# Kernel tuning notes

Hardware: AMD Instinct MI355X
Metric: run time of the kernel (lower is better)

Reference implementation:

```python
import jax, jax.numpy as jnp
import numpy as np

N_EMBD = 2560
N_HEAD = 32
HEAD_DIM = N_EMBD // N_HEAD  # 80
ROTARY_DIM = 32
SEQ = 2048
BSZ = 1


def _rope_tables(seq_len, rotary_dim, base=10000.0):
    inv_freq = 1.0 / (base ** (np.arange(0, rotary_dim, 2, dtype=np.float32) / rotary_dim))
    t = np.arange(seq_len, dtype=np.float32)
    freqs = np.outer(t, inv_freq)                      # [S, rd/2]
    emb = np.concatenate([freqs, freqs], axis=-1)      # [S, rd]
    return jnp.asarray(np.cos(emb)), jnp.asarray(np.sin(emb))


def setup_inputs() -> dict:
    key = jax.random.key(0)
    k1, k2, k3, k4, k5 = jax.random.split(key, 5)
    op_size = HEAD_DIM * (N_HEAD + 2 * N_HEAD)  # fused q,k,v => 3*n_embd
    hidden_states = jax.random.normal(k1, (BSZ, SEQ, N_EMBD), dtype=jnp.float32)
    Wqkv_w = jax.random.normal(k2, (op_size, N_EMBD), dtype=jnp.float32) * 0.02
    Wqkv_b = jax.random.normal(k3, (op_size,), dtype=jnp.float32) * 0.02
    out_w = jax.random.normal(k4, (N_EMBD, N_EMBD), dtype=jnp.float32) * 0.02
    out_b = jax.random.normal(k5, (N_EMBD,), dtype=jnp.float32) * 0.02
    cos, sin = _rope_tables(SEQ, ROTARY_DIM)
    return {"hidden_states": hidden_states, "Wqkv_w": Wqkv_w, "Wqkv_b": Wqkv_b,
            "out_w": out_w, "out_b": out_b, "cos": cos, "sin": sin}


def apply_partial_rotary(x, cos, sin):
    # x: [S, B, H, D]; cos/sin: [S, rd]
    rd = cos.shape[-1]
    c = cos[:, None, None, :]
    s = sin[:, None, None, :]
    x_rot = x[..., :rd]
    # NOTE: faithful to source -- rotated half is concatenated WITHOUT negation
    tmp = jnp.concatenate([x[..., rd // 2:rd], x[..., :rd // 2]], axis=-1)
    rotten = x_rot * c + tmp * s
    return jnp.concatenate([rotten, x[..., rd:]], axis=-1)


def reference(hidden_states, Wqkv_w, Wqkv_b, out_w, out_b, cos, sin):
    bsz, q_len, _ = hidden_states.shape
    qkv = hidden_states @ Wqkv_w.T + Wqkv_b            # [B, S, 3*E]
    q, k, v = jnp.split(qkv, 3, axis=-1)
    # [B, S, H, D] -> [S, B, H, D] for rotary
    q = q.reshape(bsz, q_len, N_HEAD, HEAD_DIM).transpose(1, 0, 2, 3)
    k = k.reshape(bsz, q_len, N_HEAD, HEAD_DIM).transpose(1, 0, 2, 3)
    v = v.reshape(bsz, q_len, N_HEAD, HEAD_DIM).transpose(0, 2, 1, 3)  # [B, H, S, D]
    cos_t, sin_t = cos[:q_len], sin[:q_len]
    q = apply_partial_rotary(q, cos_t, sin_t).transpose(1, 2, 0, 3)    # [B, H, S, D]
    k = apply_partial_rotary(k, cos_t, sin_t).transpose(1, 2, 0, 3)    # [B, H, S, D]
    scale = 1.0 / jnp.sqrt(jnp.asarray(HEAD_DIM, dtype=q.dtype))
    scores = jnp.einsum('bhqd,bhkd->bhqk', q, k) * scale
    causal = jnp.tril(jnp.ones((q_len, q_len), dtype=bool))
    scores = jnp.where(causal, scores, jnp.asarray(-1e30, dtype=scores.dtype))
    probs = jax.nn.softmax(scores, axis=-1)
    out = jnp.einsum('bhqk,bhkd->bhqd', probs, v)       # [B, H, S, D]
    out = out.transpose(0, 2, 1, 3).reshape(bsz, q_len, N_EMBD)
    return out @ out_w.T + out_b
```

## Files before the change

kernel.cpp:

```cpp
#include <hip/hip_runtime.h>
#include <cstdint>
#include <cstddef>

typedef unsigned short bf16_t;
typedef __attribute__((ext_vector_type(8))) short bf16x8;
typedef __attribute__((ext_vector_type(4))) float f32x4;

__device__ __forceinline__ float bf2f(bf16_t b) {
  unsigned int u = ((unsigned int)b) << 16;
  return __builtin_bit_cast(float, u);
}
__device__ __forceinline__ bf16_t f2bf(float f) {
  unsigned int u = __builtin_bit_cast(unsigned int, f);
  u += 0x7fffu + ((u >> 16) & 1u);
  return (bf16_t)(u >> 16);
}
__device__ __forceinline__ float exp2_hw(float x) {
  return __builtin_amdgcn_exp2f(x);
}

constexpr int SEQ = 2048, NE = 2560, NH = 32, HD = 80, OP = 7680;

__global__ void cvt3(const float* __restrict__ s0, const float* __restrict__ s1,
                     const float* __restrict__ s2, bf16_t* __restrict__ d0,
                     bf16_t* __restrict__ d1, bf16_t* __restrict__ d2)
{
  constexpr int N0 = SEQ * NE / 4, N1 = OP * NE / 4;
  int t = blockIdx.x * 256 + threadIdx.x;
  const float* s; bf16_t* d;
  if (t < N0)            { s = s0; d = d0; }
  else if (t < N0 + N1)  { s = s1; d = d1; t -= N0; }
  else                   { s = s2; d = d2; t -= N0 + N1; }
  float4 v = ((const float4*)s)[t];
  ushort4 o;
  o.x = f2bf(v.x); o.y = f2bf(v.y); o.z = f2bf(v.z); o.w = f2bf(v.w);
  ((ushort4*)d)[t] = o;
}

__device__ __forceinline__ void store_out(bf16_t* p, float v) { *p = f2bf(v); }
__device__ __forceinline__ void store_out(float* p, float v)  { *p = v; }

__global__ __launch_bounds__(512, 2) void gemm256_bt_bias(
    const bf16_t* __restrict__ A,
    const bf16_t* __restrict__ B,
    const float*  __restrict__ bias,
    bf16_t* __restrict__ C,
    int M, int N, int K)
{
  __shared__ bf16_t As[2][256 * 64];
  __shared__ bf16_t Bs[2][256 * 64];

  const int tid  = threadIdx.x;
  const int lane = tid & 63;
  const int wave = tid >> 6;
  const int wm   = wave >> 2;
  const int wn   = wave & 3;
  const int lm   = lane & 15;
  const int quad = lane >> 4;
  const int m0 = blockIdx.y * 256;
  const int n0 = blockIdx.x * 256;
  const int NT = K / 64;

  const int srow = lane >> 3;
  const int scol = ((lane & 7) ^ srow) * 8;

  auto stage = [&](const bf16_t* __restrict__ P, int R0, int K0, int H, bf16_t* DST) {
#pragma unroll
    for (int cc = 0; cc < 2; ++cc) {
      const int seg = wave * 2 + cc;
      const bf16_t* src = P + (size_t)(R0 + H * 128 + seg * 8 + srow) * K + K0 + scol;
      __builtin_amdgcn_global_load_lds(
          (const __attribute__((address_space(1))) unsigned int*)src,
          (__attribute__((address_space(3))) unsigned int*)(DST + H * 8192 + seg * 512),
          16, 0, 0);
    }
  };

  const int xk0 = ((0 + quad) ^ (lm & 7)) * 8;
  const int xk1 = ((4 + quad) ^ (lm & 7)) * 8;

  f32x4 acc[8][4];
#pragma unroll
  for (int i = 0; i < 8; ++i)
#pragma unroll
    for (int j = 0; j < 4; ++j)
      acc[i][j] = (f32x4){0.f, 0.f, 0.f, 0.f};

  stage(A, m0, 0, 0, As[0]);  stage(A, m0, 0, 1, As[0]);
  stage(B, n0, 0, 0, Bs[0]);  stage(B, n0, 0, 1, Bs[0]);
  stage(B, n0, 64, 0, Bs[1]); stage(B, n0, 64, 1, Bs[1]);
  stage(A, m0, 64, 0, As[1]); stage(A, m0, 64, 1, As[1]);

  for (int t = 0; t < NT; ++t) {
    const int c = t & 1;
    const bf16_t* Ab = &As[c][(wm * 128 + lm) * 64];
    const bf16_t* Bb = &Bs[c][(wn * 64 + lm) * 64];

    if (t == NT - 1) asm volatile("s_waitcnt vmcnt(0)" ::: "memory");
    else             asm volatile("s_waitcnt vmcnt(8)" ::: "memory");
    __builtin_amdgcn_s_barrier();

    bf16x8 a[4][2], b01[2][2], b23[2][2];

#pragma unroll
    for (int i = 0; i < 4; ++i) {
      a[i][0] = *(const bf16x8*)(Ab + i * 1024 + xk0);
      a[i][1] = *(const bf16x8*)(Ab + i * 1024 + xk1);
    }
#pragma unroll
    for (int j = 0; j < 2; ++j) {
      b01[j][0] = *(const bf16x8*)(Bb + j * 1024 + xk0);
      b01[j][1] = *(const bf16x8*)(Bb + j * 1024 + xk1);
    }
    __builtin_amdgcn_s_barrier();
    asm volatile("s_waitcnt lgkmcnt(0)" ::: "memory");
    __builtin_amdgcn_sched_barrier(0);
    __builtin_amdgcn_s_setprio(1);
#pragma unroll
    for (int kk = 0; kk < 2; ++kk)
#pragma unroll
      for (int i = 0; i < 4; ++i)
#pragma unroll
        for (int j = 0; j < 2; ++j)
          acc[i][j] = __builtin_amdgcn_mfma_f32_16x16x32_bf16(a[i][kk], b01[j][kk], acc[i][j], 0, 0, 0);
    __builtin_amdgcn_s_setprio(0);
    __builtin_amdgcn_s_barrier();

#pragma unroll
    for (int j = 0; j < 2; ++j) {
      b23[j][0] = *(const bf16x8*)(Bb + (2 + j) * 1024 + xk0);
      b23[j][1] = *(const bf16x8*)(Bb + (2 + j) * 1024 + xk1);
    }
    __builtin_amdgcn_s_barrier();
    asm volatile("s_waitcnt lgkmcnt(0)" ::: "memory");
    __builtin_amdgcn_sched_barrier(0);
    __builtin_amdgcn_s_setprio(1);
#pragma unroll
    for (int kk = 0; kk < 2; ++kk)
#pragma unroll
      for (int i = 0; i < 4; ++i)
#pragma unroll
        for (int j = 0; j < 2; ++j)
          acc[i][2 + j] = __builtin_amdgcn_mfma_f32_16x16x32_bf16(a[i][kk], b23[j][kk], acc[i][2 + j], 0, 0, 0);
    __builtin_amdgcn_s_setprio(0);
    __builtin_amdgcn_s_barrier();

#pragma unroll
    for (int i = 0; i < 4; ++i) {
      a[i][0] = *(const bf16x8*)(Ab + (4 + i) * 1024 + xk0);
      a[i][1] = *(const bf16x8*)(Ab + (4 + i) * 1024 + xk1);
    }
    if (t + 2 < NT) {
      stage(B, n0, (t + 2) * 64, 0, (bf16_t*)Bs[c]);
      stage(B, n0, (t + 2) * 64, 1, (bf16_t*)Bs[c]);
    }
    __builtin_amdgcn_s_barrier();
    asm volatile("s_waitcnt lgkmcnt(0)" ::: "memory");
    __builtin_amdgcn_sched_barrier(0);
    __builtin_amdgcn_s_setprio(1);
#pragma unroll
    for (int kk = 0; kk < 2; ++kk)
#pragma unroll
      for (int i = 0; i < 4; ++i)
#pragma unroll
        for (int j = 0; j < 2; ++j)
          acc[4 + i][j] = __builtin_amdgcn_mfma_f32_16x16x32_bf16(a[i][kk], b01[j][kk], acc[4 + i][j], 0, 0, 0);
    __builtin_amdgcn_s_setprio(0);
    __builtin_amdgcn_s_barrier();

    if (t + 2 < NT) {
      stage(A, m0, (t + 2) * 64, 0, (bf16_t*)As[c]);
      stage(A, m0, (t + 2) * 64, 1, (bf16_t*)As[c]);
    }
    __builtin_amdgcn_s_barrier();
    __builtin_amdgcn_s_setprio(1);
#pragma unroll
    for (int kk = 0; kk < 2; ++kk)
#pragma unroll
      for (int i = 0; i < 4; ++i)
#pragma unroll
        for (int j = 0; j < 2; ++j)
          acc[4 + i][2 + j] = __builtin_amdgcn_mfma_f32_16x16x32_bf16(a[i][kk], b23[j][kk], acc[4 + i][2 + j], 0, 0, 0);
    __builtin_amdgcn_s_setprio(0);
  }

#pragma unroll
  for (int i = 0; i < 8; ++i) {
#pragma unroll
    for (int j = 0; j < 4; ++j) {
      const int n = n0 + wn * 64 + j * 16 + lm;
      const float bv = bias ? bias[n] : 0.f;
#pragma unroll
      for (int r = 0; r < 4; ++r) {
        const int m = m0 + wm * 128 + i * 16 + quad * 4 + r;
        C[(size_t)m * N + n] = f2bf(acc[i][j][r] + bv);
      }
    }
  }
}

template <typename OutT>
__global__ __launch_bounds__(256, 2) void gemm_bt_bias(
    const bf16_t* __restrict__ A,
    const bf16_t* __restrict__ B,
    const float*  __restrict__ bias,
    OutT* __restrict__ C,
    int M, int N, int K, int klen)
{
  __shared__ bf16_t As[2][128 * 32];
  __shared__ bf16_t Bs[2][128 * 32];

  const int tid  = threadIdx.x;
  const int lane = tid & 63;
  const int wave = tid >> 6;
  const int m0 = blockIdx.y * 128;
  const int n0 = blockIdx.x * 128;
  const int kbeg = blockIdx.z * klen;
  OutT* Cz = C + (size_t)blockIdx.z * M * N;
  const int mw = (wave >> 1) * 64;
  const int nw = (wave & 1) * 64;
  const int lm = lane & 15;
  const int lq = lane >> 4;

  f32x4 acc[4][4];
#pragma unroll
  for (int i = 0; i < 4; ++i)
#pragma unroll
    for (int j = 0; j < 4; ++j)
      acc[i][j] = (f32x4){0.f, 0.f, 0.f, 0.f};

  const int ldr = lane >> 2;
  const int ldc = (lane & 3) * 8;

  for (int kt = kbeg; kt < kbeg + klen; kt += 64) {
#pragma unroll
    for (int sub = 0; sub < 2; ++sub) {
#pragma unroll
      for (int r = 0; r < 2; ++r) {
        const int seg = wave * 2 + r;
        const int row = seg * 16 + ldr;
        const int col = kt + sub * 32 + ldc;
        const bf16_t* ga = A + (size_t)(m0 + row) * K + col;
        const bf16_t* gb = B + (size_t)(n0 + row) * K + col;
        __builtin_amdgcn_global_load_lds(
            (const __attribute__((address_space(1))) unsigned int*)ga,
            (__attribute__((address_space(3))) unsigned int*)&As[sub][seg * 512], 16, 0, 0);
        __builtin_amdgcn_global_load_lds(
            (const __attribute__((address_space(1))) unsigned int*)gb,
            (__attribute__((address_space(3))) unsigned int*)&Bs[sub][seg * 512], 16, 0, 0);
      }
    }
    __syncthreads();

#pragma unroll
    for (int sub = 0; sub < 2; ++sub) {
      bf16x8 af[4], bfq[4];
#pragma unroll
      for (int i = 0; i < 4; ++i)
        af[i] = *(const bf16x8*)&As[sub][(mw + i * 16 + lm) * 32 + lq * 8];
#pragma unroll
      for (int j = 0; j < 4; ++j)
        bfq[j] = *(const bf16x8*)&Bs[sub][(nw + j * 16 + lm) * 32 + lq * 8];

#pragma unroll
      for (int i = 0; i < 4; ++i)
#pragma unroll
        for (int j = 0; j < 4; ++j)
          acc[i][j] = __builtin_amdgcn_mfma_f32_16x16x32_bf16(af[i], bfq[j], acc[i][j], 0, 0, 0);
    }

    __syncthreads();
  }

#pragma unroll
  for (int i = 0; i < 4; ++i) {
#pragma unroll
    for (int j = 0; j < 4; ++j) {
      const int n = n0 + nw + j * 16 + lm;
      const float bv = bias ? bias[n] : 0.f;
#pragma unroll
      for (int r = 0; r < 4; ++r) {
        const int m = m0 + mw + i * 16 + lq * 4 + r;
        store_out(&Cz[(size_t)m * N + n], acc[i][j][r] + bv);
      }
    }
  }
}

__global__ void reduce2_bias(const float* __restrict__ p, const float* __restrict__ bias,
                             float* __restrict__ out)
{
  const int t = blockIdx.x * 256 + threadIdx.x;
  const float4 a = ((const float4*)p)[t];
  const float4 b = ((const float4*)(p + (size_t)SEQ * NE))[t];
  const float4 bv = ((const float4*)bias)[t % (NE / 4)];
  float4 r;
  r.x = a.x + b.x + bv.x; r.y = a.y + b.y + bv.y;
  r.z = a.z + b.z + bv.z; r.w = a.w + b.w + bv.w;
  ((float4*)out)[t] = r;
}

constexpr int TSTR = 82;
__global__ void rope_vtrans(bf16_t* __restrict__ qkv,
                            const float* __restrict__ cosb,
                            const float* __restrict__ sinb,
                            bf16_t* __restrict__ vtg)
{
  __shared__ bf16_t T[64 * TSTR];
  const int tid = threadIdx.x;

  if (blockIdx.x < 8192) {
    const int t = blockIdx.x * 256 + tid;
    const int i  = t & 15;
    const int qk = (t >> 4) & 1;
    const int h  = (t >> 5) & 31;
    const int s  = t >> 10;
    const size_t base = (size_t)s * OP + qk * NE + h * HD;
    const float xi = bf2f(qkv[base + i]);
    const float xj = bf2f(qkv[base + i + 16]);
    const float c1 = cosb[s * 32 + i];
    const float s1 = sinb[s * 32 + i];
    const float c2 = cosb[s * 32 + i + 16];
    const float s2 = sinb[s * 32 + i + 16];
    qkv[base + i]      = f2bf(xi * c1 + xj * s1);
    qkv[base + i + 16] = f2bf(xj * c2 + xi * s2);
    return;
  }

  const int vb = blockIdx.x - 8192;
  const int h  = vb >> 5;
  const int sb = (vb & 31) * 64;
  const int voff = 2 * NE + h * HD;

#pragma unroll
  for (int i = 0; i < 10; ++i) {
    const int u = i * 256 + tid;
    const int row = u / 40, c = u % 40;
    const unsigned int w = *(const unsigned int*)(qkv + (size_t)(sb + row) * OP + voff + 2 * c);
    *(unsigned int*)&T[row * TSTR + 2 * c] = w;
  }
  __syncthreads();

  bf16_t* vh = vtg + (size_t)h * HD * SEQ;
#pragma unroll
  for (int i = 0; i < 10; ++i) {
    const int u = i * 256 + tid;
    const int d = u >> 5, sp = u & 31;
    const unsigned int lo = T[(2 * sp) * TSTR + d];
    const unsigned int hi = T[(2 * sp + 1) * TSTR + d];
    *(unsigned int*)(vh + (size_t)d * SEQ + sb + 2 * sp) = lo | (hi << 16);
  }
}

constexpr int KSTR = 96;
constexpr int VSTR = 72;
constexpr int PSTR = 72;

__global__ __launch_bounds__(256, 4) void attn_mfma(
    const bf16_t* __restrict__ qkv, const bf16_t* __restrict__ vtg,
    bf16_t* __restrict__ aout)
{
  __shared__ bf16_t Ks[12 * 512];
  __shared__ bf16_t Vt[12 * 512];
  __shared__ bf16_t Ps[4][16 * PSTR];

  const int h    = blockIdx.y;
  const int qt   = (int)gridDim.x - 1 - blockIdx.x;
  const int q0   = qt * 64;
  const int tid  = threadIdx.x;
  const int lane = tid & 63;
  const int wave = tid >> 6;
  const int lm   = lane & 15;
  const int quad = lane >> 4;

  const int qg = q0 + 16 * wave + lm;

  const int koff = NE + h * HD;
  const bf16_t* vh = vtg + (size_t)h * HD * SEQ;
  const float EC = 0.1118033988749895f * 1.4426950408889634f;

  bf16x8 qf[3];
  {
    const bf16_t* q_r = qkv + (size_t)qg * OP + h * HD;
#pragma unroll
    for (int ks = 0; ks < 3; ++ks) {
      const int col = ks * 32 + quad * 8;
      if (col < 80) qf[ks] = *(const bf16x8*)(q_r + col);
      else          qf[ks] = (bf16x8){0,0,0,0,0,0,0,0};
    }
  }

  int kofs[3];
#pragma unroll
  for (int r = 0; r < 3; ++r) {
    const int e = (wave * 3 + r) * 512 + lane * 8;
    const int row = e / 96, c = e % 96;
    kofs[r] = row * OP + (c < 80 ? c : c - 16);
  }
  int vofs[3];
#pragma unroll
  for (int r = 0; r < 3; ++r) {
    const int e = (wave * 3 + r) * 512 + lane * 8;
    int row = e / 72;
    const int c = e % 72;
    if (row >= 80) row -= 80;
    vofs[r] = row * SEQ + (c < 64 ? c : c - 16);
  }

  f32x4 oacc[5];
#pragma unroll
  for (int mt = 0; mt < 5; ++mt) oacc[mt] = (f32x4){0.f,0.f,0.f,0.f};
  float lsum = 0.f;

  const int ntiles = qt + 1;
  for (int t = 0; t < ntiles; ++t) {
    const int kb = t * 64;

#pragma unroll
    for (int r = 0; r < 3; ++r) {
      const bf16_t* gk = qkv + (size_t)kb * OP + koff + kofs[r];
      __builtin_amdgcn_global_load_lds(
          (const __attribute__((address_space(1))) unsigned int*)gk,
          (__attribute__((address_space(3))) unsigned int*)&Ks[(wave * 3 + r) * 512],
          16, 0, 0);
      const bf16_t* gv = vh + kb + vofs[r];
      __builtin_amdgcn_global_load_lds(
          (const __attribute__((address_space(1))) unsigned int*)gv,
          (__attribute__((address_space(3))) unsigned int*)&Vt[(wave * 3 + r) * 512],
          16, 0, 0);
    }
    __syncthreads();

    f32x4 sacc[4];
#pragma unroll
    for (int mt = 0; mt < 4; ++mt) sacc[mt] = (f32x4){0.f,0.f,0.f,0.f};
#pragma unroll
    for (int ks = 0; ks < 3; ++ks) {
      bf16x8 kf[4];
#pragma unroll
      for (int mt = 0; mt < 4; ++mt)
        kf[mt] = *(const bf16x8*)&Ks[(mt * 16 + lm) * KSTR + ks * 32 + quad * 8];
#pragma unroll
      for (int mt = 0; mt < 4; ++mt)
        sacc[mt] = __builtin_amdgcn_mfma_f32_16x16x32_bf16(kf[mt], qf[ks], sacc[mt], 0, 0, 0);
    }

    if (t == ntiles - 1) {
      const int keyb = kb + quad * 4;
#pragma unroll
      for (int mt = 0; mt < 4; ++mt) {
        float ps[4];
#pragma unroll
        for (int r = 0; r < 4; ++r) {
          float p = exp2_hw(sacc[mt][r] * EC);
          p = (keyb + mt * 16 + r > qg) ? 0.f : p;
          ps[r] = p;
        }
        lsum += (ps[0] + ps[1]) + (ps[2] + ps[3]);
        ushort4 pk;
        pk.x = f2bf(ps[0]); pk.y = f2bf(ps[1]); pk.z = f2bf(ps[2]); pk.w = f2bf(ps[3]);
        *(ushort4*)&Ps[wave][lm * PSTR + mt * 16 + quad * 4] = pk;
      }
    } else {
#pragma unroll
      for (int mt = 0; mt < 4; ++mt) {
        float ps[4];
#pragma unroll
        for (int r = 0; r < 4; ++r) ps[r] = exp2_hw(sacc[mt][r] * EC);
        lsum += (ps[0] + ps[1]) + (ps[2] + ps[3]);
        ushort4 pk;
        pk.x = f2bf(ps[0]); pk.y = f2bf(ps[1]); pk.z = f2bf(ps[2]); pk.w = f2bf(ps[3]);
        *(ushort4*)&Ps[wave][lm * PSTR + mt * 16 + quad * 4] = pk;
      }
    }

#pragma unroll
    for (int ks = 0; ks < 2; ++ks) {
      bf16x8 vf[5], pf;
#pragma unroll
      for (int mt = 0; mt < 5; ++mt)
        vf[mt] = *(const bf16x8*)&Vt[(mt * 16 + lm) * VSTR + ks * 32 + quad * 8];
      pf = *(const bf16x8*)&Ps[wave][lm * PSTR + ks * 32 + quad * 8];
#pragma unroll
      for (int mt = 0; mt < 5; ++mt)
        oacc[mt] = __builtin_amdgcn_mfma_f32_16x16x32_bf16(vf[mt], pf, oacc[mt], 0, 0, 0);
    }
    __syncthreads();
  }

  lsum += __shfl_xor(lsum, 16);
  lsum += __shfl_xor(lsum, 32);
  const float inv = 1.f / lsum;
  bf16_t* base = aout + (size_t)qg * NE + h * HD + quad * 4;
#pragma unroll
  for (int mt = 0; mt < 5; ++mt) {
    ushort4 st;
    st.x = f2bf(oacc[mt][0] * inv);
    st.y = f2bf(oacc[mt][1] * inv);
    st.z = f2bf(oacc[mt][2] * inv);
    st.w = f2bf(oacc[mt][3] * inv);
    *(ushort4*)(base + mt * 16) = st;
  }
}

extern "C" void kernel_launch(void* const* d_in, const int* in_sizes, int n_in,
                              void* d_out, int out_size, void* d_ws, size_t ws_size,
                              hipStream_t stream)
{
  const float* hs   = (const float*)d_in[0];
  const float* wqkv = (const float*)d_in[1];
  const float* bqkv = (const float*)d_in[2];
  const float* wout = (const float*)d_in[3];
  const float* bout = (const float*)d_in[4];
  const float* cosb = (const float*)d_in[5];
  const float* sinb = (const float*)d_in[6];

  bf16_t* hs_bf   = (bf16_t*)d_ws;
  bf16_t* wqkv_bf = hs_bf   + (size_t)SEQ * NE;
  bf16_t* wout_bf = wqkv_bf + (size_t)OP * NE;
  bf16_t* qkv     = wout_bf + (size_t)NE * NE;
  bf16_t* aout    = qkv     + (size_t)SEQ * OP;
  float*  out     = (float*)d_out;
  bf16_t* vtg     = hs_bf;
  float*  pbuf    = (float*)d_ws;

  constexpr int CVT_T = (SEQ * NE + OP * NE + NE * NE) / 4;
  cvt3<<<CVT_T / 256, 256, 0, stream>>>(hs, wqkv, wout, hs_bf, wqkv_bf, wout_bf);

  gemm256_bt_bias<<<dim3(OP / 256, SEQ / 256), 512, 0, stream>>>(
      hs_bf, wqkv_bf, bqkv, qkv, SEQ, OP, NE);
  rope_vtrans<<<8192 + 1024, 256, 0, stream>>>(qkv, cosb, sinb, vtg);
  attn_mfma<<<dim3(SEQ / 64, NH), 256, 0, stream>>>(qkv, vtg, aout);
  gemm_bt_bias<float><<<dim3(NE / 128, SEQ / 128, 2), 256, 0, stream>>>(
      aout, wout_bf, nullptr, pbuf, SEQ, NE, NE, NE / 2);
  reduce2_bias<<<(SEQ * NE / 4) / 256, 256, 0, stream>>>(pbuf, bout, out);
}
```

Before: 390.3 us.

## Software-pipeline LDS fragment loads in GEMM main loop and cut barriers

```diff
diff --git a/kernel.cpp b/kernel.cpp
--- a/kernel.cpp
+++ b/kernel.cpp
@@ -79,6 +79,9 @@
   const int xk0 = ((0 + quad) ^ (lm & 7)) * 8;
   const int xk1 = ((4 + quad) ^ (lm & 7)) * 8;
 
+  const int AOFF = (wm * 128 + lm) * 64;
+  const int BOFF = (wn * 64  + lm) * 64;
+
   f32x4 acc[8][4];
 #pragma unroll
   for (int i = 0; i < 8; ++i)
@@ -88,52 +91,59 @@
 
   stage(A, m0, 0, 0, As[0]);  stage(A, m0, 0, 1, As[0]);
   stage(B, n0, 0, 0, Bs[0]);  stage(B, n0, 0, 1, Bs[0]);
+  stage(A, m0, 64, 0, As[1]); stage(A, m0, 64, 1, As[1]);
   stage(B, n0, 64, 0, Bs[1]); stage(B, n0, 64, 1, Bs[1]);
-  stage(A, m0, 64, 0, As[1]); stage(A, m0, 64, 1, As[1]);
+
+  asm volatile("s_waitcnt vmcnt(8)" ::: "memory");
+  __builtin_amdgcn_s_barrier();
+  __builtin_amdgcn_sched_barrier(0);
+
+  bf16x8 a[4][2], b01[2][2], b23[2][2];
+#pragma unroll
+  for (int j = 0; j < 2; ++j) {
+    b01[j][0] = *(const bf16x8*)(&Bs[0][BOFF + j * 1024 + xk0]);
+    b01[j][1] = *(const bf16x8*)(&Bs[0][BOFF + j * 1024 + xk1]);
+  }
+#pragma unroll
+  for (int i = 0; i < 4; ++i) {
+    a[i][0] = *(const bf16x8*)(&As[0][AOFF + i * 1024 + xk0]);
+    a[i][1] = *(const bf16x8*)(&As[0][AOFF + i * 1024 + xk1]);
+  }
+  __builtin_amdgcn_sched_barrier(0);
 
   for (int t = 0; t < NT; ++t) {
     const int c = t & 1;
-    const bf16_t* Ab = &As[c][(wm * 128 + lm) * 64];
-    const bf16_t* Bb = &Bs[c][(wn * 64 + lm) * 64];
-
-    if (t == NT - 1) asm volatile("s_waitcnt vmcnt(0)" ::: "memory");
-    else             asm volatile("s_waitcnt vmcnt(8)" ::: "memory");
-    __builtin_amdgcn_s_barrier();
-
-    bf16x8 a[4][2], b01[2][2], b23[2][2];
-
-#pragma unroll
-    for (int i = 0; i < 4; ++i) {
-      a[i][0] = *(const bf16x8*)(Ab + i * 1024 + xk0);
-      a[i][1] = *(const bf16x8*)(Ab + i * 1024 + xk1);
-    }
-#pragma unroll
-    for (int j = 0; j < 2; ++j) {
-      b01[j][0] = *(const bf16x8*)(Bb + j * 1024 + xk0);
-      b01[j][1] = *(const bf16x8*)(Bb + j * 1024 + xk1);
-    }
-    __builtin_amdgcn_s_barrier();
-    asm volatile("s_waitcnt lgkmcnt(0)" ::: "memory");
-    __builtin_amdgcn_sched_barrier(0);
+    const bf16_t* Ac = &As[c][0];
+    const bf16_t* Bc = &Bs[c][0];
+    const bf16_t* An = &As[c ^ 1][0];
+    const bf16_t* Bn = &Bs[c ^ 1][0];
+
     __builtin_amdgcn_s_setprio(1);
 #pragma unroll
     for (int kk = 0; kk < 2; ++kk)
 #pragma unroll
-      for (int i = 0; i < 4; ++i)
+      for (int i = 0; i < 2; ++i)
 #pragma unroll
         for (int j = 0; j < 2; ++j)
           acc[i][j] = __builtin_amdgcn_mfma_f32_16x16x32_bf16(a[i][kk], b01[j][kk], acc[i][j], 0, 0, 0);
     __builtin_amdgcn_s_setprio(0);
-    __builtin_amdgcn_s_barrier();
-
 #pragma unroll
     for (int j = 0; j < 2; ++j) {
-      b23[j][0] = *(const bf16x8*)(Bb + (2 + j) * 1024 + xk0);
-      b23[j][1] = *(const bf16x8*)(Bb + (2 + j) * 1024 + xk1);
-    }
-    __builtin_amdgcn_s_barrier();
-    asm volatile("s_waitcnt lgkmcnt(0)" ::: "memory");
-    __builtin_amdgcn_sched_barrier(0);
+      b23[j][0] = *(const bf16x8*)(Bc + BOFF + (2 + j) * 1024 + xk0);
+      b23[j][1] = *(const bf16x8*)(Bc + BOFF + (2 + j) * 1024 + xk1);
+    }
+    __builtin_amdgcn_sched_barrier(0);
+    __builtin_amdgcn_s_setprio(1);
+#pragma unroll
+    for (int kk = 0; kk < 2; ++kk)
+#pragma unroll
+      for (int i = 2; i < 4; ++i)
+#pragma unroll
+        for (int j = 0; j < 2; ++j)
+          acc[i][j] = __builtin_amdgcn_mfma_f32_16x16x32_bf16(a[i][kk], b01[j][kk], acc[i][j], 0, 0, 0);
+    __builtin_amdgcn_s_setprio(0);
+    __builtin_amdgcn_sched_barrier(0);
+
     __builtin_amdgcn_s_setprio(1);
 #pragma unroll
     for (int kk = 0; kk < 2; ++kk)
@@ -143,45 +153,60 @@
         for (int j = 0; j < 2; ++j)
           acc[i][2 + j] = __builtin_amdgcn_mfma_f32_16x16x32_bf16(a[i][kk], b23[j][kk], acc[i][2 + j], 0, 0, 0);
     __builtin_amdgcn_s_setprio(0);
+#pragma unroll
+    for (int i = 0; i < 4; ++i) {
+      a[i][0] = *(const bf16x8*)(Ac + AOFF + 4096 + i * 1024 + xk0);
+      a[i][1] = *(const bf16x8*)(Ac + AOFF + 4096 + i * 1024 + xk1);
+    }
+    __builtin_amdgcn_sched_barrier(0);
+
+    __builtin_amdgcn_s_setprio(1);
+#pragma unroll
+    for (int kk = 0; kk < 2; ++kk)
+#pragma unroll
+      for (int i = 0; i < 4; ++i)
+#pragma unroll
+        for (int j = 0; j < 2; ++j)
+          acc[4 + i][j] = __builtin_amdgcn_mfma_f32_16x16x32_bf16(a[i][kk], b01[j][kk], acc[4 + i][j], 0, 0, 0);
+    __builtin_amdgcn_s_setprio(0);
+    __builtin_amdgcn_sched_barrier(0);
+
+    asm volatile("s_waitcnt lgkmcnt(0)" ::: "memory");
+    asm volatile("s_waitcnt vmcnt(0)"  ::: "memory");
     __builtin_amdgcn_s_barrier();
-
-#pragma unroll
-    for (int i = 0; i < 4; ++i) {
-      a[i][0] = *(const bf16x8*)(Ab + (4 + i) * 1024 + xk0);
-      a[i][1] = *(const bf16x8*)(Ab + (4 + i) * 1024 + xk1);
-    }
+    __builtin_amdgcn_sched_barrier(0);
+    if (t + 1 < NT) {
+#pragma unroll
+      for (int j = 0; j < 2; ++j) {
+        b01[j][0] = *(const bf16x8*)(Bn + BOFF + j * 1024 + xk0);
+        b01[j][1] = *(const bf16x8*)(Bn + BOFF + j * 1024 + xk1);
+      }
+    }
+    __builtin_amdgcn_sched_barrier(0);
+
+    __builtin_amdgcn_s_setprio(1);
+#pragma unroll
+    for (int kk = 0; kk < 2; ++kk)
+#pragma unroll
+      for (int i = 0; i < 4; ++i)
+#pragma unroll
+        for (int j = 0; j < 2; ++j)
+          acc[4 + i][2 + j] = __builtin_amdgcn_mfma_f32_16x16x32_bf16(a[i][kk], b23[j][kk], acc[4 + i][2 + j], 0, 0, 0);
+    __builtin_amdgcn_s_setprio(0);
     if (t + 2 < NT) {
       stage(B, n0, (t + 2) * 64, 0, (bf16_t*)Bs[c]);
       stage(B, n0, (t + 2) * 64, 1, (bf16_t*)Bs[c]);
-    }
-    __builtin_amdgcn_s_barrier();
-    asm volatile("s_waitcnt lgkmcnt(0)" ::: "memory");
-    __builtin_amdgcn_sched_barrier(0);
-    __builtin_amdgcn_s_setprio(1);
-#pragma unroll
-    for (int kk = 0; kk < 2; ++kk)
-#pragma unroll
-      for (int i = 0; i < 4; ++i)
-#pragma unroll
-        for (int j = 0; j < 2; ++j)
-          acc[4 + i][j] = __builtin_amdgcn_mfma_f32_16x16x32_bf16(a[i][kk], b01[j][kk], acc[4 + i][j], 0, 0, 0);
-    __builtin_amdgcn_s_setprio(0);
-    __builtin_amdgcn_s_barrier();
-
-    if (t + 2 < NT) {
       stage(A, m0, (t + 2) * 64, 0, (bf16_t*)As[c]);
       stage(A, m0, (t + 2) * 64, 1, (bf16_t*)As[c]);
     }
-    __builtin_amdgcn_s_barrier();
-    __builtin_amdgcn_s_setprio(1);
-#pragma unroll
-    for (int kk = 0; kk < 2; ++kk)
-#pragma unroll
-      for (int i = 0; i < 4; ++i)
-#pragma unroll
-        for (int j = 0; j < 2; ++j)
-          acc[4 + i][2 + j] = __builtin_amdgcn_mfma_f32_16x16x32_bf16(a[i][kk], b23[j][kk], acc[4 + i][2 + j], 0, 0, 0);
-    __builtin_amdgcn_s_setprio(0);
+    if (t + 1 < NT) {
+#pragma unroll
+      for (int i = 0; i < 4; ++i) {
+        a[i][0] = *(const bf16x8*)(An + AOFF + i * 1024 + xk0);
+        a[i][1] = *(const bf16x8*)(An + AOFF + i * 1024 + xk1);
+      }
+    }
+    __builtin_amdgcn_sched_barrier(0);
   }
 
 #pragma unroll
```

Result: faster. 381.6 us (-2.2%).
